# Performance work log

Measured on AMD Instinct MI355X. Metric: run time of the kernel, lower is better.

## Reference

```python
import jax, jax.numpy as jnp
import numpy as np

NUM_CLASSES = 256
WEIGHT = 0.0005
EPS = 1e-12  # torch F.normalize eps


def setup_inputs() -> dict:
    key = jax.random.key(0)
    k1, k2 = jax.random.split(key)
    features = jax.random.normal(k1, (32768, 1024), dtype=jnp.float32)
    labels = jax.random.randint(k2, (32768,), 0, NUM_CLASSES, dtype=jnp.int32)
    return {"features": features, "labels": labels}


def _centroid_loss(features, labels):
    B, D = features.shape
    # row-wise L2 normalize (torch F.normalize: x / max(||x||, eps))
    norms = jnp.linalg.norm(features, axis=1, keepdims=True)
    f = features / jnp.maximum(norms, EPS)

    ones = jnp.ones((B,), f.dtype)
    counts = jax.ops.segment_sum(ones, labels, num_segments=NUM_CLASSES)  # [C]
    sums = jax.ops.segment_sum(f, labels, num_segments=NUM_CLASSES)       # [C, D]

    # rank of each sample within its class (order of first appearance),
    # matching the row order of features[class_mask] in the original loop
    onehot = jax.nn.one_hot(labels, NUM_CLASSES, dtype=jnp.int32)          # [B, C]
    rank = jnp.take_along_axis(jnp.cumsum(onehot, axis=0), labels[:, None].astype(jnp.int32), axis=1)[:, 0] - 1

    # idx_table[c, r] = global index of the r-th member of class c; sentinel B if none
    idx_table = jnp.full((NUM_CLASSES, B), B, dtype=jnp.int32)
    idx_table = idx_table.at[labels, rank].set(jnp.arange(B, dtype=jnp.int32))

    # NOTE: the original code indexes class_features with the GLOBAL index i
    # (arange(n_c) != i), i.e. it excludes the member of the class at position i,
    # and excludes nothing when i >= n_c. We reproduce that exactly.
    arange_b = jnp.arange(B)
    k = idx_table[labels, arange_b]            # class member at in-class position i (global i)
    valid_excl = k < B                          # exclusion only happens when i < class size
    excl_feat = jnp.where(valid_excl[:, None], f[jnp.where(valid_excl, k, 0)], 0.0)

    n_c = counts[labels]                        # class size per sample (float)
    denom = jnp.where(valid_excl, n_c - 1.0, n_c)
    denom = jnp.maximum(denom, 1.0)             # safe for masked-out singleton classes
    centroid = (sums[labels] - excl_feat) / denom[:, None]

    dist = jnp.mean((f - centroid) ** 2, axis=1)  # F.mse_loss(..., reduction='mean')
    contrib = jnp.where(n_c > 1.0, dist, 0.0)     # skip classes with <=1 sample
    return WEIGHT * jnp.sum(contrib) / B


def reference(features, labels):
    return _centroid_loss(features, labels)
```

## Files before the change

### kernel.cpp

```cpp
#include <hip/hip_runtime.h>

#define BN 32768
#define DN 1024
#define CN 256
#define RCAP 512
#define FPAD 192
#define SUBS 8

__device__ __forceinline__ float dot4(float4 a, float4 b) {
    return a.x*b.x + a.y*b.y + a.z*b.z + a.w*b.w;
}

__global__ void __launch_bounds__(256) kc_compact(const int* __restrict__ labels,
                                                  int* __restrict__ idx,
                                                  int* __restrict__ counts,
                                                  float* __restrict__ acc) {
    __shared__ unsigned int packed[BN / 4];
    __shared__ int wcnt[4];
    const int c = blockIdx.x;
    const int t = threadIdx.x;

    for (int w = t; w < BN / 4; w += 256) {
        const int4 v = ((const int4*)labels)[w];
        packed[w] = (unsigned int)(v.x & 255)
                  | ((unsigned int)(v.y & 255) << 8)
                  | ((unsigned int)(v.z & 255) << 16)
                  | ((unsigned int)(v.w & 255) << 24);
    }
    __syncthreads();

    const int wave = t >> 6, lane = t & 63;
    const unsigned long long lt = (lane == 0) ? 0ull : (~0ull >> (64 - lane));
    const int ch0 = wave * 128, ch1 = ch0 + 128;

    int cnt = 0;
    for (int ch = ch0; ch < ch1; ++ch) {
        const int gi = ch * 64 + lane;
        const int lab = (packed[gi >> 2] >> ((gi & 3) * 8)) & 255;
        cnt += __popcll(__ballot(lab == c));
    }
    if (lane == 0) wcnt[wave] = cnt;
    __syncthreads();

    int base = 0;
    for (int w2 = 0; w2 < wave; ++w2) base += wcnt[w2];

    for (int ch = ch0; ch < ch1; ++ch) {
        const int gi = ch * 64 + lane;
        const int lab = (packed[gi >> 2] >> ((gi & 3) * 8)) & 255;
        const bool pred = (lab == c);
        const unsigned long long mask = __ballot(pred);
        if (pred) {
            const int pos = base + __popcll(mask & lt);
            if (pos < RCAP) idx[c * RCAP + pos] = gi;
        }
        base += __popcll(mask);
    }
    if (t == 0) {
        counts[c] = wcnt[0] + wcnt[1] + wcnt[2] + wcnt[3];
        if (c == 0) *acc = 0.0f;
    }
}

__global__ void __launch_bounds__(256) k_rnorm(const float4* __restrict__ x4,
                                               float* __restrict__ rnorm) {
    const int wave = threadIdx.x >> 6;
    const int lane = threadIdx.x & 63;
    const int row = blockIdx.x * 4 + wave;
    const float4* base = x4 + (size_t)row * (DN / 4);
    const float4 v0 = base[lane];
    const float4 v1 = base[lane + 64];
    const float4 v2 = base[lane + 128];
    const float4 v3 = base[lane + 192];
    float ss = dot4(v0, v0) + dot4(v1, v1) + dot4(v2, v2) + dot4(v3, v3);
#pragma unroll
    for (int off = 32; off; off >>= 1) ss += __shfl_xor(ss, off, 64);
    if (lane == 0) rnorm[row] = 1.0f / fmaxf(sqrtf(ss), 1e-12f);
}

__global__ void __launch_bounds__(256, 4) k_gather3(const float4* __restrict__ x4,
                                                    const int* __restrict__ idx,
                                                    const int* __restrict__ counts,
                                                    const float* __restrict__ rnorm,
                                                    float4* __restrict__ partials) {
    __shared__ int sic[RCAP];
    __shared__ float srn[RCAP];
    const int b = blockIdx.x;
    const int c = b >> 3;
    const int sub = b & 7;
    const int t = threadIdx.x;

    const int nn = min(counts[c], RCAP);

    if (t < FPAD) {
        const int r = (t < nn) ? t : 0;
        const int row = idx[c * RCAP + r];
        sic[t] = row;
        srn[t] = (t < nn) ? rnorm[row] : 0.0f;
    }
    const int nnpad = min((nn + 31) & ~31, RCAP);
    for (int i = FPAD + t; i < nnpad; i += 256) {
        const int row = idx[c * RCAP + i];
        sic[i] = row;
        srn[i] = rnorm[row];
    }
    __syncthreads();

    int rows[6][4];
#pragma unroll
    for (int j = 0; j < 6; ++j) {
        const int rb = j * 32 + sub * 4;
#pragma unroll
        for (int k = 0; k < 4; ++k) rows[j][k] = sic[rb + k];
    }

    float4 acc = make_float4(0.f, 0.f, 0.f, 0.f);
#pragma unroll
    for (int j = 0; j < 6; ++j) {
        const int rb = j * 32 + sub * 4;
#pragma unroll
        for (int k = 0; k < 4; ++k) {
            const float4 v = x4[(size_t)rows[j][k] * 256 + t];
            const float rn = srn[rb + k];
            acc.x += v.x * rn; acc.y += v.y * rn;
            acc.z += v.z * rn; acc.w += v.w * rn;
        }
    }
    for (int rb = FPAD + sub * 4; rb < nnpad; rb += 32) {
#pragma unroll
        for (int k = 0; k < 4; ++k) {
            const float4 v = x4[(size_t)sic[rb + k] * 256 + t];
            const float rn = srn[rb + k];
            acc.x += v.x * rn; acc.y += v.y * rn;
            acc.z += v.z * rn; acc.w += v.w * rn;
        }
    }
    partials[(size_t)b * 256 + t] = acc;
}

__global__ void __launch_bounds__(256) k_red(const float4* __restrict__ partials,
                                             const int* __restrict__ counts,
                                             float* __restrict__ sums,
                                             float* __restrict__ snorm2,
                                             float* __restrict__ acc) {
    __shared__ float wred[4];
    const int c = blockIdx.x;
    const int t = threadIdx.x;
    const int wave = t >> 6, lane = t & 63;

    float4 tot = make_float4(0.f, 0.f, 0.f, 0.f);
#pragma unroll
    for (int s = 0; s < SUBS; ++s) {
        const float4 p = partials[(size_t)(c * SUBS + s) * 256 + t];
        tot.x += p.x; tot.y += p.y; tot.z += p.z; tot.w += p.w;
    }
    ((float4*)sums)[(size_t)c * 256 + t] = tot;

    float d = dot4(tot, tot);
#pragma unroll
    for (int off = 32; off; off >>= 1) d += __shfl_xor(d, off, 64);
    if (lane == 0) wred[wave] = d;
    __syncthreads();
    if (t == 0) {
        const float s2 = wred[0] + wred[1] + wred[2] + wred[3];
        snorm2[c] = s2;
        const int n = counts[c];
        if (n > 1) {
            const float nf = (float)n;
            atomicAdd(acc, (nf - s2 / nf) * (1.0f / DN));
        }
    }
}

__global__ void __launch_bounds__(256) k_corr(const float4* __restrict__ x4,
                                              const int* __restrict__ labels,
                                              const int* __restrict__ counts,
                                              const int* __restrict__ idx,
                                              const float* __restrict__ rnorm,
                                              const float* __restrict__ sums,
                                              const float* __restrict__ snorm2,
                                              float* __restrict__ acc) {
    const int i = blockIdx.x;
    const int c = labels[i];
    const int n = counts[c];
    if (i >= n || n < 2 || i >= RCAP) return;
    const int k = idx[c * RCAP + i];
    const int t = threadIdx.x;

    const float4 xi = x4[(size_t)i * 256 + t];
    const float4 xk = x4[(size_t)k * 256 + t];
    const float4 s  = ((const float4*)sums)[(size_t)c * 256 + t];

    float d0 = dot4(xi, s);
    float d1 = dot4(xi, xk);
    float d2 = dot4(xk, s);
    float d3 = dot4(xk, xk);
#pragma unroll
    for (int off = 32; off; off >>= 1) {
        d0 += __shfl_xor(d0, off, 64);
        d1 += __shfl_xor(d1, off, 64);
        d2 += __shfl_xor(d2, off, 64);
        d3 += __shfl_xor(d3, off, 64);
    }
    __shared__ float4 wred[4];
    if ((t & 63) == 0) wred[t >> 6] = make_float4(d0, d1, d2, d3);
    __syncthreads();
    if (t == 0) {
        const float xiS  = wred[0].x + wred[1].x + wred[2].x + wred[3].x;
        const float xixk = wred[0].y + wred[1].y + wred[2].y + wred[3].y;
        const float xkS  = wred[0].z + wred[1].z + wred[2].z + wred[3].z;
        const float xkxk = wred[0].w + wred[1].w + wred[2].w + wred[3].w;
        const float rni = rnorm[i], rnk = rnorm[k], s2 = snorm2[c];
        const float fiS  = rni * xiS;
        const float fifk = rni * rnk * xixk;
        const float Sfk  = rnk * xkS;
        const float fk2  = rnk * rnk * xkxk;
        const float nf = (float)n;
        const float dd = nf - 1.0f;
        const float naive = -2.0f * fiS / nf + s2 / (nf * nf);
        const float corr  = -2.0f * (fiS - fifk) / dd + (s2 - 2.0f * Sfk + fk2) / (dd * dd);
        atomicAdd(acc, (corr - naive) * (1.0f / DN));
    }
}

__global__ void k_fin(const float* __restrict__ acc, float* __restrict__ out) {
    out[0] = (0.0005f / (float)BN) * acc[0];
}

extern "C" void kernel_launch(void* const* d_in, const int* in_sizes, int n_in,
                              void* d_out, int out_size, void* d_ws, size_t ws_size,
                              hipStream_t stream) {
    const float* features = (const float*)d_in[0];
    const int* labels = (const int*)d_in[1];
    float* out = (float*)d_out;

    char* ws = (char*)d_ws;
    float4* partials = (float4*)(ws + 0);
    float*  rnorm    = (float*)(ws + 8388608);
    float*  sums     = (float*)(ws + 8519680);
    int*    idx      = (int*)  (ws + 9568256);
    int*    counts   = (int*)  (ws + 10092544);
    float*  snorm2   = (float*)(ws + 10093568);
    float*  acc      = (float*)(ws + 10094592);

    const float4* x4 = (const float4*)features;

    kc_compact<<<CN, 256, 0, stream>>>(labels, idx, counts, acc);
    k_rnorm<<<BN / 4, 256, 0, stream>>>(x4, rnorm);
    k_gather3<<<CN * SUBS, 256, 0, stream>>>(x4, idx, counts, rnorm, partials);
    k_red<<<CN, 256, 0, stream>>>(partials, counts, sums, snorm2, acc);
    k_corr<<<RCAP, 256, 0, stream>>>(x4, labels, counts, idx, rnorm, sums, snorm2, acc);
    k_fin<<<1, 1, 0, stream>>>(acc, out);
}
```

Before: 237.7 us.

## Fuse row-norm computation into class gather kernel with wave-per-row accumulation

Measured after the change: 241.7 us. Within noise of the previous version (+1.7%).

```diff
diff --git a/kernel.cpp b/kernel.cpp
--- a/kernel.cpp
+++ b/kernel.cpp
@@ -62,80 +62,97 @@
     }
 }
 
-__global__ void __launch_bounds__(256) k_rnorm(const float4* __restrict__ x4,
-                                               float* __restrict__ rnorm) {
-    const int wave = threadIdx.x >> 6;
-    const int lane = threadIdx.x & 63;
-    const int row = blockIdx.x * 4 + wave;
-    const float4* base = x4 + (size_t)row * (DN / 4);
-    const float4 v0 = base[lane];
-    const float4 v1 = base[lane + 64];
-    const float4 v2 = base[lane + 128];
-    const float4 v3 = base[lane + 192];
-    float ss = dot4(v0, v0) + dot4(v1, v1) + dot4(v2, v2) + dot4(v3, v3);
-#pragma unroll
-    for (int off = 32; off; off >>= 1) ss += __shfl_xor(ss, off, 64);
-    if (lane == 0) rnorm[row] = 1.0f / fmaxf(sqrtf(ss), 1e-12f);
-}
-
-__global__ void __launch_bounds__(256, 4) k_gather3(const float4* __restrict__ x4,
-                                                    const int* __restrict__ idx,
-                                                    const int* __restrict__ counts,
-                                                    const float* __restrict__ rnorm,
-                                                    float4* __restrict__ partials) {
-    __shared__ int sic[RCAP];
-    __shared__ float srn[RCAP];
+__global__ void __launch_bounds__(256, 3) k_fused(const float4* __restrict__ x4,
+                                                  const int* __restrict__ idx,
+                                                  const int* __restrict__ counts,
+                                                  float* __restrict__ rnorm,
+                                                  float4* __restrict__ partials) {
+    __shared__ int sic[FPAD];
+    __shared__ float facc[(DN / 4) * 5];
     const int b = blockIdx.x;
     const int c = b >> 3;
     const int sub = b & 7;
     const int t = threadIdx.x;
-
+    const int wave = t >> 6, lane = t & 63;
     const int nn = min(counts[c], RCAP);
 
-    if (t < FPAD) {
-        const int r = (t < nn) ? t : 0;
-        const int row = idx[c * RCAP + r];
-        sic[t] = row;
-        srn[t] = (t < nn) ? rnorm[row] : 0.0f;
-    }
-    const int nnpad = min((nn + 31) & ~31, RCAP);
-    for (int i = FPAD + t; i < nnpad; i += 256) {
-        const int row = idx[c * RCAP + i];
-        sic[i] = row;
-        srn[i] = rnorm[row];
-    }
-    __syncthreads();
-
-    int rows[6][4];
+    if (t < FPAD) sic[t] = (nn > 0) ? idx[c * RCAP + min(t, nn - 1)] : 0;
+    for (int i = t; i < (DN / 4) * 5; i += 256) facc[i] = 0.0f;
+    __syncthreads();
+
+    const int ws = (sub << 2) | wave;
+    int rows[6];
+#pragma unroll
+    for (int j = 0; j < 6; ++j) rows[j] = sic[ws + 32 * j];
+
+    float4 v[6][4];
+    float p[6];
 #pragma unroll
     for (int j = 0; j < 6; ++j) {
-        const int rb = j * 32 + sub * 4;
-#pragma unroll
-        for (int k = 0; k < 4; ++k) rows[j][k] = sic[rb + k];
-    }
-
-    float4 acc = make_float4(0.f, 0.f, 0.f, 0.f);
+        const float4* rb = x4 + (size_t)rows[j] * 256;
+        v[j][0] = rb[lane];
+        v[j][1] = rb[lane + 64];
+        v[j][2] = rb[lane + 128];
+        v[j][3] = rb[lane + 192];
+        p[j] = dot4(v[j][0], v[j][0]) + dot4(v[j][1], v[j][1])
+             + dot4(v[j][2], v[j][2]) + dot4(v[j][3], v[j][3]);
+    }
+
+    float rn[6];
 #pragma unroll
     for (int j = 0; j < 6; ++j) {
-        const int rb = j * 32 + sub * 4;
-#pragma unroll
-        for (int k = 0; k < 4; ++k) {
-            const float4 v = x4[(size_t)rows[j][k] * 256 + t];
-            const float rn = srn[rb + k];
-            acc.x += v.x * rn; acc.y += v.y * rn;
-            acc.z += v.z * rn; acc.w += v.w * rn;
-        }
-    }
-    for (int rb = FPAD + sub * 4; rb < nnpad; rb += 32) {
-#pragma unroll
-        for (int k = 0; k < 4; ++k) {
-            const float4 v = x4[(size_t)sic[rb + k] * 256 + t];
-            const float rn = srn[rb + k];
-            acc.x += v.x * rn; acc.y += v.y * rn;
-            acc.z += v.z * rn; acc.w += v.w * rn;
-        }
-    }
-    partials[(size_t)b * 256 + t] = acc;
+        float ss = p[j];
+#pragma unroll
+        for (int off = 32; off; off >>= 1) ss += __shfl_xor(ss, off, 64);
+        const float r = 1.0f / fmaxf(sqrtf(ss), 1e-12f);
+        const bool valid = (ws + 32 * j) < nn;
+        rn[j] = valid ? r : 0.0f;
+        if (valid && lane == 0) rnorm[rows[j]] = r;
+    }
+
+    float4 a[4];
+    a[0] = a[1] = a[2] = a[3] = make_float4(0.f, 0.f, 0.f, 0.f);
+#pragma unroll
+    for (int j = 0; j < 6; ++j) {
+#pragma unroll
+        for (int q = 0; q < 4; ++q) {
+            a[q].x += v[j][q].x * rn[j];
+            a[q].y += v[j][q].y * rn[j];
+            a[q].z += v[j][q].z * rn[j];
+            a[q].w += v[j][q].w * rn[j];
+        }
+    }
+
+    if (nn > FPAD) {
+        for (int s = FPAD + ws; s < nn; s += 32) {
+            const int row = idx[c * RCAP + s];
+            const float4* rb = x4 + (size_t)row * 256;
+            const float4 w0 = rb[lane], w1 = rb[lane + 64];
+            const float4 w2 = rb[lane + 128], w3 = rb[lane + 192];
+            float ss = dot4(w0, w0) + dot4(w1, w1) + dot4(w2, w2) + dot4(w3, w3);
+#pragma unroll
+            for (int off = 32; off; off >>= 1) ss += __shfl_xor(ss, off, 64);
+            const float r = 1.0f / fmaxf(sqrtf(ss), 1e-12f);
+            if (lane == 0) rnorm[row] = r;
+            a[0].x += w0.x * r; a[0].y += w0.y * r; a[0].z += w0.z * r; a[0].w += w0.w * r;
+            a[1].x += w1.x * r; a[1].y += w1.y * r; a[1].z += w1.z * r; a[1].w += w1.w * r;
+            a[2].x += w2.x * r; a[2].y += w2.y * r; a[2].z += w2.z * r; a[2].w += w2.w * r;
+            a[3].x += w3.x * r; a[3].y += w3.y * r; a[3].z += w3.z * r; a[3].w += w3.w * r;
+        }
+    }
+
+#pragma unroll
+    for (int q = 0; q < 4; ++q) {
+        const int qq = lane + q * 64;
+        atomicAdd(&facc[5 * qq + 0], a[q].x);
+        atomicAdd(&facc[5 * qq + 1], a[q].y);
+        atomicAdd(&facc[5 * qq + 2], a[q].z);
+        atomicAdd(&facc[5 * qq + 3], a[q].w);
+    }
+    __syncthreads();
+
+    partials[(size_t)b * 256 + t] = make_float4(facc[5 * t + 0], facc[5 * t + 1],
+                                                facc[5 * t + 2], facc[5 * t + 3]);
 }
 
 __global__ void __launch_bounds__(256) k_red(const float4* __restrict__ partials,
@@ -246,8 +263,7 @@
     const float4* x4 = (const float4*)features;
 
     kc_compact<<<CN, 256, 0, stream>>>(labels, idx, counts, acc);
-    k_rnorm<<<BN / 4, 256, 0, stream>>>(x4, rnorm);
-    k_gather3<<<CN * SUBS, 256, 0, stream>>>(x4, idx, counts, rnorm, partials);
+    k_fused<<<CN * SUBS, 256, 0, stream>>>(x4, idx, counts, rnorm, partials);
     k_red<<<CN, 256, 0, stream>>>(partials, counts, sums, snorm2, acc);
     k_corr<<<RCAP, 256, 0, stream>>>(x4, labels, counts, idx, rnorm, sums, snorm2, acc);
     k_fin<<<1, 1, 0, stream>>>(acc, out);
```
